# Kernel optimization log

Measured on AMD Instinct MI355X. Metric: run time of the kernel, lower is better.

Reference implementation:

```python
import jax, jax.numpy as jnp
import numpy as np

DECAY = 0.99
EPS = 1e-05


def setup_inputs() -> dict:
    key = jax.random.key(0)
    k1, k2 = jax.random.split(key)
    B, C, H, W = 16, 64, 64, 64
    dim, n_embed = 64, 2048
    x = jax.random.normal(k1, (B, C, H, W), dtype=jnp.float32)
    embed = jax.random.normal(k2, (dim, n_embed), dtype=jnp.float32)
    cluster_size = jnp.zeros((n_embed,), dtype=jnp.float32)
    embed_avg = embed.copy()
    return {"x": x, "embed": embed, "cluster_size": cluster_size, "embed_avg": embed_avg}


def reference(x, embed, cluster_size, embed_avg):
    # x: [B, C, H, W], embed: [dim, n_embed]
    dim, n_embed = embed.shape
    xp = jnp.transpose(x, (0, 2, 3, 1))            # [B, H, W, dim]
    flat = xp.reshape(-1, dim)                     # [N, dim]

    # Pairwise squared distances: ||f||^2 - 2 f.E + ||e||^2  -> [N, n_embed]
    dist = (jnp.sum(flat * flat, axis=1, keepdims=True)
            - 2.0 * (flat @ embed)
            + jnp.sum(embed * embed, axis=0, keepdims=True))
    embed_ind_flat = jnp.argmin(dist, axis=1)      # [N]

    # Gather codes (embed_code)
    quantize = embed.T[embed_ind_flat].reshape(xp.shape)  # [B, H, W, dim]
    embed_ind = embed_ind_flat.reshape(xp.shape[:-1])     # [B, H, W]

    # Training-mode EMA codebook update (functional; buffers returned)
    counts = jax.ops.segment_sum(jnp.ones_like(embed_ind_flat, dtype=flat.dtype),
                                 embed_ind_flat, num_segments=n_embed)      # onehot.sum(0)
    embed_sum = jax.ops.segment_sum(flat, embed_ind_flat,
                                    num_segments=n_embed).T                 # flat.T @ onehot -> [dim, n_embed]
    new_cluster_size = DECAY * cluster_size + (1.0 - DECAY) * counts
    new_embed_avg = DECAY * embed_avg + (1.0 - DECAY) * embed_sum
    n = jnp.sum(new_cluster_size)
    cs = (new_cluster_size + EPS) / (n + n_embed * EPS) * n
    new_embed = new_embed_avg / cs[None, :]

    diff = jnp.mean((jax.lax.stop_gradient(quantize) - xp) ** 2)
    quantize_st = xp + jax.lax.stop_gradient(quantize - xp)
    out = jnp.transpose(quantize_st, (0, 3, 1, 2))  # back to NCHW
    return out, diff, embed_ind, new_embed, new_cluster_size, new_embed_avg
```

## Files before the change

### kernel.cpp

```cpp
#include <hip/hip_runtime.h>
#include <stdint.h>

#define DIM 64
#define NE 2048
#define NROWS 65536
#define HW 4096

#define DECAYF 0.99f
#define OMDF ((float)(1.0 - 0.99))
#define EPSF 1e-5f
#define NEPSF ((float)(2048.0 * 1e-5))

typedef _Float16 f16x8 __attribute__((ext_vector_type(8)));
typedef float f32x4 __attribute__((ext_vector_type(4)));

#define SPLIT_SCALE 1024.0f
#define SPLIT_INV 0.0009765625f

__global__ __launch_bounds__(256) void prep_kernel(const float* __restrict__ E,
                                                   _Float16* __restrict__ Eh,
                                                   _Float16* __restrict__ El,
                                                   float* __restrict__ se) {
  const int bid = blockIdx.x;
  const int tid = threadIdx.x;
  if (bid < 64) {
    int task = bid * 256 + tid;
    int l = task & 63;
    int ks = (task >> 6) & 1;
    int t = task >> 7;
    int j = t * 16 + (l & 15);
    int d0 = ks * 32 + ((l >> 4) & 3) * 8;
    _Float16 h8[8], l8[8];
#pragma unroll
    for (int r = 0; r < 8; ++r) {
      float v = E[(d0 + r) * NE + j];
      _Float16 h = (_Float16)v;
      h8[r] = h;
      l8[r] = (_Float16)((v - (float)h) * SPLIT_SCALE);
    }
    *(f16x8*)(Eh + (size_t)task * 8) = *(f16x8*)h8;
    *(f16x8*)(El + (size_t)task * 8) = *(f16x8*)l8;
  } else {
    int j = (bid - 64) * 256 + tid;
    float s = 0.f;
#pragma unroll
    for (int d = 0; d < DIM; ++d) {
      float v = E[d * NE + j];
      s += v * v;
    }
    se[j] = s;
  }
}

#define MFMA16(A, B, C) __builtin_amdgcn_mfma_f32_16x16x32_f16(A, B, C, 0, 0, 0)

#define COMPUTE_TILE(T, B0, B1, B2, B3, SEJ)                              \
  {                                                                       \
    _Pragma("unroll") for (int rt = 0; rt < 2; ++rt) {                    \
      f32x4 acc1 = {0.f, 0.f, 0.f, 0.f};                                  \
      f32x4 acc2 = {0.f, 0.f, 0.f, 0.f};                                  \
      acc1 = MFMA16(xh[rt][0], B0, acc1);                                 \
      acc1 = MFMA16(xh[rt][1], B1, acc1);                                 \
      acc2 = MFMA16(xh[rt][0], B2, acc2);                                 \
      acc2 = MFMA16(xh[rt][1], B3, acc2);                                 \
      acc2 = MFMA16(xl[rt][0], B0, acc2);                                 \
      acc2 = MFMA16(xl[rt][1], B1, acc2);                                 \
      _Pragma("unroll") for (int q = 0; q < 4; ++q) {                     \
        float dot = fmaf(acc2[q], SPLIT_INV, acc1[q]);                    \
        float dist = fmaf(-2.f, dot, SEJ);                                \
        if (dist < bv[rt][q]) { bv[rt][q] = dist; bi[rt][q] = (T)*16 + lc; } \
      }                                                                   \
    }                                                                     \
  }

__global__ __launch_bounds__(256) void argmin_mfma_kernel(
    const float* __restrict__ x, const _Float16* __restrict__ Eh,
    const _Float16* __restrict__ El, const float* __restrict__ se,
    int* __restrict__ ind, float* __restrict__ ind_f) {
  const int tid = threadIdx.x;
  const int lane = tid & 63;
  const int wv = tid >> 6;
  const int R0 = blockIdx.x * 128 + wv * 32;
  const int lg = (lane >> 4) & 3;
  const int lc = lane & 15;

  f16x8 xh[2][2], xl[2][2];
#pragma unroll
  for (int rt = 0; rt < 2; ++rt) {
#pragma unroll
    for (int ks = 0; ks < 2; ++ks) {
      int r_glob = R0 + rt * 16 + lc;
      const float* xr = x + (size_t)(r_glob >> 12) * (DIM * HW) + (r_glob & 4095);
      int d0 = ks * 32 + lg * 8;
      _Float16 h8[8], l8[8];
#pragma unroll
      for (int e = 0; e < 8; ++e) {
        float v = xr[(d0 + e) * HW];
        _Float16 h = (_Float16)v;
        h8[e] = h;
        l8[e] = (_Float16)((v - (float)h) * SPLIT_SCALE);
      }
      xh[rt][ks] = *(f16x8*)h8;
      xl[rt][ks] = *(f16x8*)l8;
    }
  }

  float bv[2][4];
  int bi[2][4];
#pragma unroll
  for (int rt = 0; rt < 2; ++rt)
#pragma unroll
    for (int q = 0; q < 4; ++q) { bv[rt][q] = 3.4e38f; bi[rt][q] = 0; }

  const size_t lo = (size_t)lane * 8;
  f16x8 c0 = *(const f16x8*)(Eh + lo);
  f16x8 c1 = *(const f16x8*)(Eh + 512 + lo);
  f16x8 c2 = *(const f16x8*)(El + lo);
  f16x8 c3 = *(const f16x8*)(El + 512 + lo);
  float seC = se[lc];

  for (int t = 0; t < NE / 16; t += 2) {
    f16x8 n0 = *(const f16x8*)(Eh + (size_t)(t + 1) * 1024 + lo);
    f16x8 n1 = *(const f16x8*)(Eh + (size_t)(t + 1) * 1024 + 512 + lo);
    f16x8 n2 = *(const f16x8*)(El + (size_t)(t + 1) * 1024 + lo);
    f16x8 n3 = *(const f16x8*)(El + (size_t)(t + 1) * 1024 + 512 + lo);
    float seN = se[(t + 1) * 16 + lc];

    COMPUTE_TILE(t, c0, c1, c2, c3, seC);

    if (t + 2 < NE / 16) {
      c0 = *(const f16x8*)(Eh + (size_t)(t + 2) * 1024 + lo);
      c1 = *(const f16x8*)(Eh + (size_t)(t + 2) * 1024 + 512 + lo);
      c2 = *(const f16x8*)(El + (size_t)(t + 2) * 1024 + lo);
      c3 = *(const f16x8*)(El + (size_t)(t + 2) * 1024 + 512 + lo);
      seC = se[(t + 2) * 16 + lc];
    }

    COMPUTE_TILE(t + 1, n0, n1, n2, n3, seN);
  }

#pragma unroll
  for (int rt = 0; rt < 2; ++rt) {
#pragma unroll
    for (int q = 0; q < 4; ++q) {
      float v = bv[rt][q];
      int ix = bi[rt][q];
#pragma unroll
      for (int off = 1; off < 16; off <<= 1) {
        float ov = __shfl_xor(v, off, 64);
        int oi = __shfl_xor(ix, off, 64);
        if (ov < v || (ov == v && oi < ix)) { v = ov; ix = oi; }
      }
      if (lc == 0) {
        int grow = R0 + rt * 16 + lg * 4 + q;
        ind[grow] = ix;
        ind_f[grow] = (float)ix;
      }
    }
  }
}

__global__ __launch_bounds__(256) void esum_fused_kernel(const float* __restrict__ x,
                                                         const float* __restrict__ E,
                                                         const int* __restrict__ ind,
                                                         float* __restrict__ out,
                                                         float* __restrict__ diff_acc,
                                                         float* __restrict__ pesum,
                                                         int* __restrict__ pcnt) {
  const int d = blockIdx.x >> 2;
  const int bg = blockIdx.x & 3;
  __shared__ float h[4][NE];
  __shared__ int cnt[NE];
  const int tid = threadIdx.x;
  const int w = tid >> 6;
  float* hf = &h[0][0];
#pragma unroll
  for (int u = 0; u < 32; ++u) hf[u * 256 + tid] = 0.f;
  if (d == 0) {
#pragma unroll
    for (int u = 0; u < 8; ++u) cnt[u * 256 + tid] = 0;
  }
  __syncthreads();
  const float* Ed = E + d * NE;
  float local = 0.f;
  for (int b = bg * 4; b < bg * 4 + 4; ++b) {
    const int* ib = ind + b * 4096;
    const float* xb = x + ((size_t)b * DIM + d) * 4096;
    float* ob = out + ((size_t)b * DIM + d) * 4096;
#pragma unroll 4
    for (int it = 0; it < 16; ++it) {
      int i = it * 256 + tid;
      int idx = ib[i];
      float xv = xb[i];
      float qv = Ed[idx];
      float dq = qv - xv;
      ob[i] = xv + dq;
      local += dq * dq;
      atomicAdd(&h[w][idx], xv);
      if (d == 0) atomicAdd(&cnt[idx], 1);
    }
  }
#pragma unroll
  for (int off = 32; off > 0; off >>= 1) local += __shfl_down(local, off, 64);
  __shared__ float wsum[4];
  if ((tid & 63) == 0) wsum[tid >> 6] = local;
  __syncthreads();
  if (tid == 0) {
    float s = (wsum[0] + wsum[1]) + (wsum[2] + wsum[3]);
    atomicAdd(diff_acc, s * (1.f / 4194304.f));
  }
  float* pe = pesum + ((size_t)bg * DIM + d) * NE;
#pragma unroll
  for (int u = 0; u < 8; ++u) {
    int j = u * 256 + tid;
    pe[j] = (h[0][j] + h[1][j]) + (h[2][j] + h[3][j]);
  }
  if (d == 0) {
    int* pc = pcnt + bg * NE;
#pragma unroll
    for (int u = 0; u < 8; ++u) {
      int j = u * 256 + tid;
      pc[j] = cnt[j];
    }
  }
}

__global__ __launch_bounds__(1024) void finalize_a4(const float* __restrict__ cs_in,
                                                    const int* __restrict__ pcnt,
                                                    float* __restrict__ ncs_slot,
                                                    float* __restrict__ n_out) {
  const int t = threadIdx.x;
  float local = 0.f;
#pragma unroll
  for (int u = 0; u < 2; ++u) {
    int k = u * 1024 + t;
    int c = (pcnt[k] + pcnt[NE + k]) + (pcnt[2 * NE + k] + pcnt[3 * NE + k]);
    float v = DECAYF * cs_in[k] + OMDF * (float)c;
    ncs_slot[k] = v;
    local += v;
  }
#pragma unroll
  for (int off = 32; off > 0; off >>= 1) local += __shfl_down(local, off, 64);
  __shared__ float red[16];
  if ((t & 63) == 0) red[t >> 6] = local;
  __syncthreads();
  if (t == 0) {
    float s = 0.f;
#pragma unroll
    for (int k = 0; k < 16; ++k) s += red[k];
    *n_out = s;
  }
}

__global__ __launch_bounds__(256) void finalize_b4(const float* __restrict__ ea_in,
                                                   const float* __restrict__ pesum,
                                                   const float* __restrict__ ncs_slot,
                                                   const float* __restrict__ n_out,
                                                   float* __restrict__ nea_slot,
                                                   float* __restrict__ ne_slot) {
  const int k = blockIdx.x * 256 + threadIdx.x;
  const float n = *n_out;
  const size_t P = (size_t)DIM * NE;
  float es = (pesum[k] + pesum[P + k]) + (pesum[2 * P + k] + pesum[3 * P + k]);
  float nea = DECAYF * ea_in[k] + OMDF * es;
  nea_slot[k] = nea;
  float ncs = ncs_slot[k & (NE - 1)];
  float cs = (ncs + EPSF) / (n + NEPSF) * n;
  ne_slot[k] = nea / cs;
}

#define BRF 128
#define TCF 128
#define NTF (NE / TCF)
__global__ __launch_bounds__(256, 2) void argmin_lds_kernel(const float* __restrict__ x,
                                                            const float* __restrict__ E,
                                                            const float* __restrict__ se,
                                                            int* __restrict__ ind,
                                                            float* __restrict__ ind_f) {
  __shared__ float Xs[DIM][BRF];
  __shared__ float Es[DIM][TCF];
  const int tid = threadIdx.x;
  const int rg = tid >> 4;
  const int cg = tid & 15;
  const int B0 = blockIdx.x * BRF;
  const float* xb = x + (size_t)(B0 >> 12) * (DIM * HW) + (B0 & 4095);
  float* Xf = &Xs[0][0];
#pragma unroll
  for (int k = 0; k < 8; ++k) {
    int i = k * 1024 + tid * 4;
    *(float4*)(Xf + i) = *(const float4*)(xb + (i >> 7) * HW + (i & 127));
  }
  float bv[8];
  int bi[8];
#pragma unroll
  for (int i2 = 0; i2 < 8; ++i2) { bv[i2] = 3.4e38f; bi[i2] = 0; }
  float* Ef = &Es[0][0];
  for (int t = 0; t < NTF; ++t) {
    __syncthreads();
#pragma unroll
    for (int k = 0; k < 8; ++k) {
      int i = k * 1024 + tid * 4;
      *(float4*)(Ef + i) = *(const float4*)(E + (i >> 7) * NE + t * TCF + (i & 127));
    }
    __syncthreads();
    float acc[8][8];
#pragma unroll
    for (int i2 = 0; i2 < 8; ++i2)
#pragma unroll
      for (int j = 0; j < 8; ++j) acc[i2][j] = 0.f;
#pragma unroll 8
    for (int d = 0; d < DIM; ++d) {
      float4 xa = *(const float4*)&Xs[d][rg * 8];
      float4 xc = *(const float4*)&Xs[d][rg * 8 + 4];
      float4 ea = *(const float4*)&Es[d][cg * 4];
      float4 ec = *(const float4*)&Es[d][cg * 4 + 64];
      float xr[8] = {xa.x, xa.y, xa.z, xa.w, xc.x, xc.y, xc.z, xc.w};
      float er[8] = {ea.x, ea.y, ea.z, ea.w, ec.x, ec.y, ec.z, ec.w};
#pragma unroll
      for (int i2 = 0; i2 < 8; ++i2)
#pragma unroll
        for (int j = 0; j < 8; ++j) acc[i2][j] = fmaf(xr[i2], er[j], acc[i2][j]);
    }
    float4 s0 = *(const float4*)(se + t * TCF + cg * 4);
    float4 s1 = *(const float4*)(se + t * TCF + cg * 4 + 64);
    float sv[8] = {s0.x, s0.y, s0.z, s0.w, s1.x, s1.y, s1.z, s1.w};
#pragma unroll
    for (int i2 = 0; i2 < 8; ++i2) {
#pragma unroll
      for (int j = 0; j < 8; ++j) {
        float dist = fmaf(-2.f, acc[i2][j], sv[j]);
        if (dist < bv[i2]) {
          bv[i2] = dist;
          bi[i2] = t * TCF + (j >> 2) * 64 + cg * 4 + (j & 3);
        }
      }
    }
  }
#pragma unroll
  for (int i2 = 0; i2 < 8; ++i2) {
    float v = bv[i2];
    int ix = bi[i2];
#pragma unroll
    for (int off = 1; off < 16; off <<= 1) {
      float ov = __shfl_xor(v, off, 64);
      int oi = __shfl_xor(ix, off, 64);
      if (ov < v || (ov == v && oi < ix)) { v = ov; ix = oi; }
    }
    bv[i2] = v;
    bi[i2] = ix;
  }
  if (cg == 0) {
#pragma unroll
    for (int i2 = 0; i2 < 8; ++i2) {
      int grow = B0 + rg * 8 + i2;
      ind[grow] = bi[i2];
      ind_f[grow] = (float)bi[i2];
    }
  }
}

__global__ __launch_bounds__(256) void outdiff_kernel(const float* __restrict__ x,
                                                      const float* __restrict__ E,
                                                      const int* __restrict__ ind,
                                                      float* __restrict__ out,
                                                      float* __restrict__ diff_acc) {
  const int t = threadIdx.x;
  float local = 0.f;
  const int base = blockIdx.x * 1024;
#pragma unroll
  for (int u = 0; u < 4; ++u) {
    int i = base + u * 256 + t;
    int hw = i & 4095;
    int bc = i >> 12;
    int c = bc & 63;
    int b = bc >> 6;
    int idx = ind[b * 4096 + hw];
    float xv = x[i];
    float qv = E[c * NE + idx];
    float dq = qv - xv;
    out[i] = xv + dq;
    local += dq * dq;
  }
#pragma unroll
  for (int off = 32; off > 0; off >>= 1) local += __shfl_down(local, off, 64);
  __shared__ float wsum[4];
  if ((t & 63) == 0) wsum[t >> 6] = local;
  __syncthreads();
  if (t == 0) {
    float s = wsum[0] + wsum[1] + wsum[2] + wsum[3];
    atomicAdd(diff_acc, s * (1.f / 4194304.f));
  }
}

__global__ __launch_bounds__(256) void scatter_atomic_kernel(const float* __restrict__ x,
                                                             const int* __restrict__ ind,
                                                             float* __restrict__ counts,
                                                             float* __restrict__ esum) {
  const int row = blockIdx.x * 256 + threadIdx.x;
  const int idx = ind[row];
  atomicAdd(&counts[idx], 1.f);
  const int b = row >> 12;
  const int hw = row & 4095;
  const float* xr = x + (size_t)b * (DIM * HW) + hw;
#pragma unroll
  for (int d = 0; d < DIM; ++d) atomicAdd(&esum[d * NE + idx], xr[d * HW]);
}

__global__ __launch_bounds__(1024) void finalize_a_float(const float* __restrict__ cs_in,
                                                         float* __restrict__ ncs_slot,
                                                         float* __restrict__ n_out) {
  const int t = threadIdx.x;
  float local = 0.f;
#pragma unroll
  for (int u = 0; u < 2; ++u) {
    int k = u * 1024 + t;
    float v = DECAYF * cs_in[k] + OMDF * ncs_slot[k];
    ncs_slot[k] = v;
    local += v;
  }
#pragma unroll
  for (int off = 32; off > 0; off >>= 1) local += __shfl_down(local, off, 64);
  __shared__ float red[16];
  if ((t & 63) == 0) red[t >> 6] = local;
  __syncthreads();
  if (t == 0) {
    float s = 0.f;
#pragma unroll
    for (int k = 0; k < 16; ++k) s += red[k];
    *n_out = s;
  }
}

__global__ __launch_bounds__(256) void finalize_b_inplace(const float* __restrict__ ea_in,
                                                          float* __restrict__ nea_slot,
                                                          const float* __restrict__ ncs_slot,
                                                          const float* __restrict__ n_out,
                                                          float* __restrict__ ne_slot) {
  const int k = blockIdx.x * 256 + threadIdx.x;
  const float n = *n_out;
  float nea = DECAYF * ea_in[k] + OMDF * nea_slot[k];
  nea_slot[k] = nea;
  float ncs = ncs_slot[k & (NE - 1)];
  float cs = (ncs + EPSF) / (n + NEPSF) * n;
  ne_slot[k] = nea / cs;
}

extern "C" void kernel_launch(void* const* d_in, const int* in_sizes, int n_in,
                              void* d_out, int out_size, void* d_ws, size_t ws_size,
                              hipStream_t stream) {
  const float* x = (const float*)d_in[0];
  const float* E = (const float*)d_in[1];
  const float* cs_in = (const float*)d_in[2];
  const float* ea_in = (const float*)d_in[3];
  float* out = (float*)d_out;

  const size_t O_OUT = 0;
  const size_t O_DIFF = 4194304;
  const size_t O_IND = 4194305;
  const size_t O_NE = 4259841;
  const size_t O_NCS = 4390913;
  const size_t O_NEA = 4392961;

  float* se = (float*)d_ws;
  int* ind = (int*)(se + NE);
  float* n_out = (float*)(ind + NROWS);
  int* pcnt = (int*)(n_out + 4);
  float* pesum = (float*)(pcnt + 4 * NE);
  _Float16* Ehpk = (_Float16*)pesum;
  _Float16* Elpk = Ehpk + (size_t)DIM * NE;
  const size_t need = (size_t)((char*)(pesum + 4 * (size_t)DIM * NE) - (char*)d_ws);
  const bool big_ws = ws_size >= need;

  hipMemsetAsync(out + O_DIFF, 0, 4, stream);

  if (big_ws) {
    prep_kernel<<<72, 256, 0, stream>>>(E, Ehpk, Elpk, se);
    argmin_mfma_kernel<<<NROWS / 128, 256, 0, stream>>>(x, Ehpk, Elpk, se, ind,
                                                        out + O_IND);
    esum_fused_kernel<<<DIM * 4, 256, 0, stream>>>(x, E, ind, out + O_OUT,
                                                   out + O_DIFF, pesum, pcnt);
    finalize_a4<<<1, 1024, 0, stream>>>(cs_in, pcnt, out + O_NCS, n_out);
    finalize_b4<<<DIM * NE / 256, 256, 0, stream>>>(ea_in, pesum, out + O_NCS, n_out,
                                                    out + O_NEA, out + O_NE);
  } else {
    prep_kernel<<<72, 256, 0, stream>>>(E, Ehpk, Elpk, se);
    argmin_lds_kernel<<<NROWS / BRF, 256, 0, stream>>>(x, E, se, ind, out + O_IND);
    outdiff_kernel<<<4096, 256, 0, stream>>>(x, E, ind, out + O_OUT, out + O_DIFF);
    hipMemsetAsync(out + O_NCS, 0, NE * 4, stream);
    hipMemsetAsync(out + O_NEA, 0, (size_t)DIM * NE * 4, stream);
    scatter_atomic_kernel<<<NROWS / 256, 256, 0, stream>>>(x, ind, out + O_NCS,
                                                           out + O_NEA);
    finalize_a_float<<<1, 1024, 0, stream>>>(cs_in, out + O_NCS, n_out);
    finalize_b_inplace<<<DIM * NE / 256, 256, 0, stream>>>(ea_in, out + O_NEA,
                                                           out + O_NCS, n_out,
                                                           out + O_NE);
  }
}
```

Baseline: 108.7 us.

## Precompute cluster-size total algebraically, fuse finalize kernels, widen esum batch split

Computes the total of the new cluster sizes early in the prep kernel, using the fact that the code counts always sum to the row count. This removes the single-block finalize_a kernel and merges its per-code work into one finalize kernel. The esum kernel also splits batches into 8 groups instead of 4 when workspace allows, doubling block count for better CU occupancy. The cost is more partial-sum memory traffic and LDS zeroing.

```diff
diff --git a/kernel.cpp b/kernel.cpp
--- a/kernel.cpp
+++ b/kernel.cpp
@@ -18,9 +18,11 @@
 #define SPLIT_INV 0.0009765625f
 
 __global__ __launch_bounds__(256) void prep_kernel(const float* __restrict__ E,
+                                                   const float* __restrict__ cs_in,
                                                    _Float16* __restrict__ Eh,
                                                    _Float16* __restrict__ El,
-                                                   float* __restrict__ se) {
+                                                   float* __restrict__ se,
+                                                   float* __restrict__ n_pre) {
   const int bid = blockIdx.x;
   const int tid = threadIdx.x;
   if (bid < 64) {
@@ -40,7 +42,7 @@
     }
     *(f16x8*)(Eh + (size_t)task * 8) = *(f16x8*)h8;
     *(f16x8*)(El + (size_t)task * 8) = *(f16x8*)l8;
-  } else {
+  } else if (bid < 72) {
     int j = (bid - 64) * 256 + tid;
     float s = 0.f;
 #pragma unroll
@@ -49,6 +51,19 @@
       s += v * v;
     }
     se[j] = s;
+  } else {
+    float local = 0.f;
+#pragma unroll
+    for (int u = 0; u < 8; ++u) local += cs_in[u * 256 + tid];
+#pragma unroll
+    for (int off = 32; off > 0; off >>= 1) local += __shfl_down(local, off, 64);
+    __shared__ float red[4];
+    if ((tid & 63) == 0) red[tid >> 6] = local;
+    __syncthreads();
+    if (tid == 0) {
+      float s = (red[0] + red[1]) + (red[2] + red[3]);
+      *n_pre = DECAYF * s + OMDF * (float)NROWS;
+    }
   }
 }
 
@@ -166,9 +181,11 @@
                                                          float* __restrict__ out,
                                                          float* __restrict__ diff_acc,
                                                          float* __restrict__ pesum,
-                                                         int* __restrict__ pcnt) {
-  const int d = blockIdx.x >> 2;
-  const int bg = blockIdx.x & 3;
+                                                         int* __restrict__ pcnt,
+                                                         int nbg) {
+  const int bg = blockIdx.x % nbg;
+  const int d = blockIdx.x / nbg;
+  const int nb = 16 / nbg;
   __shared__ float h[4][NE];
   __shared__ int cnt[NE];
   const int tid = threadIdx.x;
@@ -183,7 +200,7 @@
   __syncthreads();
   const float* Ed = E + d * NE;
   float local = 0.f;
-  for (int b = bg * 4; b < bg * 4 + 4; ++b) {
+  for (int b = bg * nb; b < bg * nb + nb; ++b) {
     const int* ib = ind + b * 4096;
     const float* xb = x + ((size_t)b * DIM + d) * 4096;
     float* ob = out + ((size_t)b * DIM + d) * 4096;
@@ -225,46 +242,29 @@
   }
 }
 
-__global__ __launch_bounds__(1024) void finalize_a4(const float* __restrict__ cs_in,
-                                                    const int* __restrict__ pcnt,
-                                                    float* __restrict__ ncs_slot,
-                                                    float* __restrict__ n_out) {
-  const int t = threadIdx.x;
-  float local = 0.f;
-#pragma unroll
-  for (int u = 0; u < 2; ++u) {
-    int k = u * 1024 + t;
-    int c = (pcnt[k] + pcnt[NE + k]) + (pcnt[2 * NE + k] + pcnt[3 * NE + k]);
-    float v = DECAYF * cs_in[k] + OMDF * (float)c;
-    ncs_slot[k] = v;
-    local += v;
-  }
-#pragma unroll
-  for (int off = 32; off > 0; off >>= 1) local += __shfl_down(local, off, 64);
-  __shared__ float red[16];
-  if ((t & 63) == 0) red[t >> 6] = local;
-  __syncthreads();
-  if (t == 0) {
-    float s = 0.f;
-#pragma unroll
-    for (int k = 0; k < 16; ++k) s += red[k];
-    *n_out = s;
-  }
-}
-
-__global__ __launch_bounds__(256) void finalize_b4(const float* __restrict__ ea_in,
-                                                   const float* __restrict__ pesum,
-                                                   const float* __restrict__ ncs_slot,
-                                                   const float* __restrict__ n_out,
-                                                   float* __restrict__ nea_slot,
-                                                   float* __restrict__ ne_slot) {
+__global__ __launch_bounds__(256) void finalize_fused(const float* __restrict__ ea_in,
+                                                      const float* __restrict__ cs_in,
+                                                      const float* __restrict__ pesum,
+                                                      const int* __restrict__ pcnt,
+                                                      const float* __restrict__ n_pre,
+                                                      float* __restrict__ nea_slot,
+                                                      float* __restrict__ ncs_slot,
+                                                      float* __restrict__ ne_slot,
+                                                      int nbg) {
   const int k = blockIdx.x * 256 + threadIdx.x;
-  const float n = *n_out;
+  const int kk = k & (NE - 1);
   const size_t P = (size_t)DIM * NE;
-  float es = (pesum[k] + pesum[P + k]) + (pesum[2 * P + k] + pesum[3 * P + k]);
+  float es = 0.f;
+  int c = 0;
+  for (int g = 0; g < nbg; ++g) {
+    es += pesum[(size_t)g * P + k];
+    c += pcnt[g * NE + kk];
+  }
+  const float n = *n_pre;
   float nea = DECAYF * ea_in[k] + OMDF * es;
   nea_slot[k] = nea;
-  float ncs = ncs_slot[k & (NE - 1)];
+  float ncs = DECAYF * cs_in[kk] + OMDF * (float)c;
+  if (k < NE) ncs_slot[k] = ncs;
   float cs = (ncs + EPSF) / (n + NEPSF) * n;
   ne_slot[k] = nea / cs;
 }
@@ -465,25 +465,32 @@
   int* ind = (int*)(se + NE);
   float* n_out = (float*)(ind + NROWS);
   int* pcnt = (int*)(n_out + 4);
-  float* pesum = (float*)(pcnt + 4 * NE);
+  const size_t P = (size_t)DIM * NE;
+  const size_t head = 2048 + 65536 + 4;
+  int nbg = 8;
+  size_t need = (head + (size_t)nbg * NE + (size_t)nbg * P) * 4;
+  if (ws_size < need) {
+    nbg = 4;
+    need = (head + (size_t)nbg * NE + (size_t)nbg * P) * 4;
+  }
+  const bool big_ws = ws_size >= need;
+  float* pesum = (float*)(pcnt + nbg * NE);
   _Float16* Ehpk = (_Float16*)pesum;
-  _Float16* Elpk = Ehpk + (size_t)DIM * NE;
-  const size_t need = (size_t)((char*)(pesum + 4 * (size_t)DIM * NE) - (char*)d_ws);
-  const bool big_ws = ws_size >= need;
+  _Float16* Elpk = Ehpk + P;
 
   hipMemsetAsync(out + O_DIFF, 0, 4, stream);
 
   if (big_ws) {
-    prep_kernel<<<72, 256, 0, stream>>>(E, Ehpk, Elpk, se);
+    prep_kernel<<<73, 256, 0, stream>>>(E, cs_in, Ehpk, Elpk, se, n_out);
     argmin_mfma_kernel<<<NROWS / 128, 256, 0, stream>>>(x, Ehpk, Elpk, se, ind,
                                                         out + O_IND);
-    esum_fused_kernel<<<DIM * 4, 256, 0, stream>>>(x, E, ind, out + O_OUT,
-                                                   out + O_DIFF, pesum, pcnt);
-    finalize_a4<<<1, 1024, 0, stream>>>(cs_in, pcnt, out + O_NCS, n_out);
-    finalize_b4<<<DIM * NE / 256, 256, 0, stream>>>(ea_in, pesum, out + O_NCS, n_out,
-                                                    out + O_NEA, out + O_NE);
+    esum_fused_kernel<<<DIM * nbg, 256, 0, stream>>>(x, E, ind, out + O_OUT,
+                                                     out + O_DIFF, pesum, pcnt, nbg);
+    finalize_fused<<<(int)(P / 256), 256, 0, stream>>>(ea_in, cs_in, pesum, pcnt,
+                                                       n_out, out + O_NEA,
+                                                       out + O_NCS, out + O_NE, nbg);
   } else {
-    prep_kernel<<<72, 256, 0, stream>>>(E, Ehpk, Elpk, se);
+    prep_kernel<<<73, 256, 0, stream>>>(E, cs_in, Ehpk, Elpk, se, n_out);
     argmin_lds_kernel<<<NROWS / BRF, 256, 0, stream>>>(x, E, se, ind, out + O_IND);
     outdiff_kernel<<<4096, 256, 0, stream>>>(x, E, ind, out + O_OUT, out + O_DIFF);
     hipMemsetAsync(out + O_NCS, 0, NE * 4, stream);
```

Measured after the change: 110.4 us. No clear change (+1.6%).
